# Kernel optimization log

Measured on AMD Instinct MI355X. Metric: run time of the kernel, lower is better.

The kernel has to match this reference:

```python
import jax, jax.numpy as jnp
import numpy as np

HEADS, DIM_HEAD = 8, 64
EPS = 1e-5  # torch InstanceNorm1d default


def instance_norm(t):
    # torch InstanceNorm1d(dim_head) applied to (b*h, n, d) normalizes over the
    # last dim d for each (b, h, n); affine=False, biased variance.
    mu = jnp.mean(t, axis=-1, keepdims=True)
    var = jnp.mean((t - mu) ** 2, axis=-1, keepdims=True)
    return (t - mu) * jax.lax.rsqrt(var + EPS)


def setup_inputs() -> dict:
    key = jax.random.key(0)
    k1, k2, k3, k4 = jax.random.split(key, 4)
    B, N, D = 8, 8192, 256
    inner = HEADS * DIM_HEAD  # 512
    x = jax.random.normal(k1, (B, N, D), jnp.float32)
    w_qkv = jax.random.normal(k2, (3 * inner, D), jnp.float32) / np.sqrt(D).astype(np.float32)
    w_out = jax.random.normal(k3, (D, inner), jnp.float32) / np.sqrt(inner).astype(np.float32)
    b_out = 0.01 * jax.random.normal(k4, (D,), jnp.float32)
    return {"x": x, "w_qkv": w_qkv, "w_out": w_out, "b_out": b_out}


def reference(x, w_qkv, w_out, b_out):
    B, N, _ = x.shape
    H, Dh = HEADS, DIM_HEAD
    # fused qkv projection: [B,N,3*H*Dh]
    qkv = jnp.einsum('bnd,ed->bne', x, w_qkv)
    q, k, v = jnp.split(qkv, 3, axis=-1)

    def to_heads(t):
        return t.reshape(B, N, H, Dh).transpose(0, 2, 1, 3)  # b h n d

    q, k, v = to_heads(q), to_heads(k), to_heads(v)
    # galerkin: instance-norm K and V
    k = instance_norm(k)
    v = instance_norm(v)
    # linear (non-softmax) attention: (K^T V) then Q @ (K^T V), scaled by 1/N
    dots = jnp.einsum('bhnd,bhne->bhde', k, v)            # [B,H,Dh,Dh]
    out = jnp.einsum('bhnd,bhde->bhne', q, dots) / N      # [B,H,N,Dh]
    out = out.transpose(0, 2, 1, 3).reshape(B, N, H * Dh)
    return jnp.einsum('bne,de->bnd', out, w_out) + b_out
```

## Files before the change

kernel.cpp:

```cpp
#include <hip/hip_runtime.h>
#include <hip/hip_bf16.h>
#include <stdint.h>

typedef __attribute__((ext_vector_type(8))) __bf16 bf16x8;
typedef __attribute__((ext_vector_type(8))) unsigned short ushort8_t;
typedef __attribute__((ext_vector_type(4))) unsigned short ushort4_t;
typedef __attribute__((ext_vector_type(4))) float f32x4;

#define MFMA16(a, b, c) __builtin_amdgcn_mfma_f32_16x16x32_bf16((a), (b), (c), 0, 0, 0)

static __device__ __forceinline__ unsigned short f2bf(float f) {
  union { float f; unsigned u; } v; v.f = f;
  unsigned r = v.u + 0x7fffu + ((v.u >> 16) & 1u);
  return (unsigned short)(r >> 16);
}
static __device__ __forceinline__ float bf2f(unsigned short u) {
  union { unsigned u; float f; } v; v.u = ((unsigned)u) << 16; return v.f;
}

static __device__ __forceinline__ void gld_lds16(const void* g, void* l) {
  __builtin_amdgcn_global_load_lds((const __attribute__((address_space(1))) void*)g,
                                   (__attribute__((address_space(3))) void*)l, 16, 0, 0);
}

__global__ __launch_bounds__(256) void k_convx(const float* __restrict__ x,
                                               unsigned short* __restrict__ xb) {
  size_t i = ((size_t)blockIdx.x * 256 + threadIdx.x) * 4;
  float4 v = *(const float4*)(x + i);
  ushort4_t o = { f2bf(v.x), f2bf(v.y), f2bf(v.z), f2bf(v.w) };
  *(ushort4_t*)(xb + i) = o;
}

__global__ void k_convw(const float* __restrict__ w, unsigned short* __restrict__ wb) {
  int i = (blockIdx.x * 256 + threadIdx.x) * 4;
  float4 v = *(const float4*)(w + i);
  ushort4_t o = { f2bf(v.x), f2bf(v.y), f2bf(v.z), f2bf(v.w) };
  *(ushort4_t*)(wb + i) = o;
}

__global__ void k_convo(const float* __restrict__ w, unsigned short* __restrict__ wb) {
  int i = (blockIdx.x * 256 + threadIdx.x) * 4;
  float4 v = *(const float4*)(w + i);
  ushort4_t o = { f2bf(v.x), f2bf(v.y), f2bf(v.z), f2bf(v.w) };
  *(ushort4_t*)(wb + i) = o;
}

__global__ __launch_bounds__(512) void k_fused(const unsigned short* __restrict__ xb,
                                               const unsigned short* __restrict__ wqb,
                                               float* __restrict__ partials) {
  __shared__ __align__(16) char smem[98304];
  unsigned short* As = (unsigned short*)smem;
  unsigned short* Bs = (unsigned short*)(smem + 65536);
  unsigned short* kt = (unsigned short*)smem;
  unsigned short* vt = (unsigned short*)(smem + 36864);

  const int t = threadIdx.x;
  const int w = t >> 6, lane = t & 63, lr = lane & 15, lg = lane >> 4;
  const int wr = w >> 1, wc = w & 1;

  const int id = blockIdx.x;
  const int nid = (id & 7) * 256 + (id >> 3);
  const int mt = nid >> 3, h = nid & 7;
  const long m0 = (long)mt * 256;

  const unsigned short* bk = wqb + (size_t)(512 + h * 64) * 256;
  const unsigned short* bv = wqb + (size_t)(1024 + h * 64) * 256;

  const int srl = t >> 3, sc = t & 7;
  const int swz = (sc ^ (srl & 7)) << 3;

#pragma unroll
  for (int i = 0; i < 4; ++i)
    gld_lds16(xb + (size_t)(m0 + i * 64 + srl) * 256 + swz, &As[i * 4096 + t * 8]);
  gld_lds16(bk + (size_t)srl * 256 + swz, &Bs[t * 8]);
  gld_lds16(bv + (size_t)srl * 256 + swz, &Bs[4096 + t * 8]);
  __syncthreads();

  f32x4 acc[4][4];
#pragma unroll
  for (int mb = 0; mb < 4; ++mb)
#pragma unroll
    for (int nb = 0; nb < 4; ++nb) acc[mb][nb] = f32x4{0.f, 0.f, 0.f, 0.f};

  for (int ks = 0; ks < 4; ++ks) {
    const int cur = ks & 1, nxt = cur ^ 1;
    if (ks < 3) {
      const int k0 = (ks + 1) * 64;
#pragma unroll
      for (int i = 0; i < 4; ++i)
        gld_lds16(xb + (size_t)(m0 + i * 64 + srl) * 256 + k0 + swz,
                  &As[nxt * 16384 + i * 4096 + t * 8]);
      gld_lds16(bk + (size_t)srl * 256 + k0 + swz, &Bs[nxt * 8192 + t * 8]);
      gld_lds16(bv + (size_t)srl * 256 + k0 + swz, &Bs[nxt * 8192 + 4096 + t * 8]);
    }
    bf16x8 a[4][2], b[4][2];
#pragma unroll
    for (int mb = 0; mb < 4; ++mb) {
      const int R = wr * 64 + mb * 16 + lr;
#pragma unroll
      for (int kh = 0; kh < 2; ++kh)
        a[mb][kh] = *(const bf16x8*)&As[cur * 16384 + R * 64 + ((((kh << 2) + lg) ^ (R & 7)) << 3)];
    }
#pragma unroll
    for (int nb = 0; nb < 4; ++nb) {
      const int E = wc * 64 + nb * 16 + lr;
#pragma unroll
      for (int kh = 0; kh < 2; ++kh)
        b[nb][kh] = *(const bf16x8*)&Bs[cur * 8192 + E * 64 + ((((kh << 2) + lg) ^ (E & 7)) << 3)];
    }
#pragma unroll
    for (int mb = 0; mb < 4; ++mb)
#pragma unroll
      for (int nb = 0; nb < 4; ++nb)
#pragma unroll
        for (int kh = 0; kh < 2; ++kh)
          acc[mb][nb] = MFMA16(a[mb][kh], b[nb][kh], acc[mb][nb]);
    __syncthreads();
  }

  unsigned short* dst = (wc == 0 ? kt : vt) + wr * 4608;
#pragma unroll
  for (int mb = 0; mb < 4; ++mb) {
#pragma unroll
    for (int rg = 0; rg < 4; ++rg) {
      float s1 = acc[mb][0][rg] + acc[mb][1][rg] + acc[mb][2][rg] + acc[mb][3][rg];
      float s2 = acc[mb][0][rg] * acc[mb][0][rg] + acc[mb][1][rg] * acc[mb][1][rg] +
                 acc[mb][2][rg] * acc[mb][2][rg] + acc[mb][3][rg] * acc[mb][3][rg];
      s1 += __shfl_xor(s1, 1); s2 += __shfl_xor(s2, 1);
      s1 += __shfl_xor(s1, 2); s2 += __shfl_xor(s2, 2);
      s1 += __shfl_xor(s1, 4); s2 += __shfl_xor(s2, 4);
      s1 += __shfl_xor(s1, 8); s2 += __shfl_xor(s2, 8);
      const float mean = s1 * (1.f / 64.f);
      const float rs = rsqrtf(s2 * (1.f / 64.f) - mean * mean + 1e-5f);
      const int nn = mb * 16 + lg * 4 + rg;
#pragma unroll
      for (int nb = 0; nb < 4; ++nb)
        dst[(nb * 16 + lr) * 72 + nn] = f2bf((acc[mb][nb][rg] - mean) * rs);
    }
  }
  __syncthreads();

  const int dblk = w >> 1, ep = w & 1;
  f32x4 acc2[2] = {f32x4{0.f, 0.f, 0.f, 0.f}, f32x4{0.f, 0.f, 0.f, 0.f}};
#pragma unroll
  for (int cn = 0; cn < 4; ++cn) {
#pragma unroll
    for (int ns = 0; ns < 64; ns += 32) {
      bf16x8 af = *(const bf16x8*)&kt[cn * 4608 + (dblk * 16 + lr) * 72 + ns + lg * 8];
#pragma unroll
      for (int e = 0; e < 2; ++e) {
        bf16x8 bvf = *(const bf16x8*)&vt[cn * 4608 + ((ep * 2 + e) * 16 + lr) * 72 + ns + lg * 8];
        acc2[e] = MFMA16(af, bvf, acc2[e]);
      }
    }
  }
  float* pb = partials + ((size_t)mt * 8 + h) * 4096;
#pragma unroll
  for (int e = 0; e < 2; ++e)
#pragma unroll
    for (int rg = 0; rg < 4; ++rg) {
      int d = dblk * 16 + lg * 4 + rg;
      int eo = (ep * 2 + e) * 16 + lr;
      pb[d * 64 + eo] = acc2[e][rg];
    }
}

__global__ __launch_bounds__(256) void k_mmat(const float* __restrict__ partials,
                                              const float* __restrict__ wqkv,
                                              unsigned short* __restrict__ tmpT) {
  __shared__ float dl[4096];
  __shared__ float wqls[64 * 256];
  const int bh = blockIdx.x, b = bh >> 3, h = bh & 7;
  const int t = threadIdx.x;
#pragma unroll
  for (int i = 0; i < 4; ++i) {
    int off = t * 16 + i * 4;
    f32x4 s = {0.f, 0.f, 0.f, 0.f};
    for (int c = 0; c < 32; ++c) {
      f32x4 p = *(const f32x4*)(partials + ((size_t)(b * 32 + c) * 8 + h) * 4096 + off);
      s += p;
    }
    *(f32x4*)&dl[off] = s;
  }
#pragma unroll
  for (int i = 0; i < 16; ++i) {
    int idx4 = i * 256 + t;
    int d = idx4 >> 6, c4 = idx4 & 63;
    *(f32x4*)&wqls[d * 256 + c4 * 4] =
        *(const f32x4*)(wqkv + (size_t)(h * 64 + d) * 256 + c4 * 4);
  }
  __syncthreads();
  const int k = t;
  const float scale = 1.0f / 8192.0f;
  float res[64];
  for (int e = 0; e < 64; ++e) {
    float s = 0.f;
#pragma unroll
    for (int d = 0; d < 64; ++d) s += dl[d * 64 + e] * wqls[d * 256 + k];
    res[e] = s * scale;
  }
  unsigned short* dstp = tmpT + (size_t)b * 131072 + (size_t)k * 512 + h * 64;
#pragma unroll
  for (int e8 = 0; e8 < 8; ++e8) {
    ushort8_t o;
#pragma unroll
    for (int j = 0; j < 8; ++j) o[j] = f2bf(res[e8 * 8 + j]);
    *(ushort8_t*)(dstp + e8 * 8) = o;
  }
}

__global__ __launch_bounds__(256) void k_pmat(const unsigned short* __restrict__ woutb,
                                              const unsigned short* __restrict__ tmpT,
                                              unsigned short* __restrict__ pswz) {
  const int bid = blockIdx.x;
  const int b = bid >> 2, oq = (bid >> 1) & 1, kq = bid & 1;
  const int t = threadIdx.x, w = t >> 6, lane = t & 63, lr = lane & 15, lg = lane >> 4;
  const int wr = w >> 1, wc = w & 1;
  const int ob = oq * 128 + wr * 64, kb = kq * 128 + wc * 64;
  const unsigned short* tb = tmpT + (size_t)b * 131072;

  f32x4 acc[4][4];
#pragma unroll
  for (int mb = 0; mb < 4; ++mb)
#pragma unroll
    for (int nb = 0; nb < 4; ++nb) acc[mb][nb] = f32x4{0.f, 0.f, 0.f, 0.f};

  for (int ks = 0; ks < 16; ++ks) {
    bf16x8 a[4], bb[4];
#pragma unroll
    for (int mb = 0; mb < 4; ++mb)
      a[mb] = *(const bf16x8*)(woutb + (size_t)(ob + mb * 16 + lr) * 512 + ks * 32 + lg * 8);
#pragma unroll
    for (int nb = 0; nb < 4; ++nb)
      bb[nb] = *(const bf16x8*)(tb + (size_t)(kb + nb * 16 + lr) * 512 + ks * 32 + lg * 8);
#pragma unroll
    for (int mb = 0; mb < 4; ++mb)
#pragma unroll
      for (int nb = 0; nb < 4; ++nb) acc[mb][nb] = MFMA16(a[mb], bb[nb], acc[mb][nb]);
  }

  unsigned short* pb = pswz + (size_t)b * 65536;
#pragma unroll
  for (int mb = 0; mb < 4; ++mb)
#pragma unroll
    for (int nb = 0; nb < 4; ++nb)
#pragma unroll
      for (int rg = 0; rg < 4; ++rg) {
        int o = ob + mb * 16 + lg * 4 + rg;
        int k = kb + nb * 16 + lr;
        pb[(((k >> 5) * 16 + (o >> 4)) * 64 + (o & 15) + ((k >> 3) & 3) * 16) * 8 + (k & 7)] =
            f2bf(acc[mb][nb][rg]);
      }
}

__global__ __launch_bounds__(512) void k_gemm2(const unsigned short* __restrict__ xb,
                                               const unsigned short* __restrict__ pswz,
                                               const float* __restrict__ bout,
                                               float* __restrict__ out) {
  __shared__ unsigned short As[2][128 * 64];
  const int b = blockIdx.x >> 6, mt = blockIdx.x & 63;
  const long m0 = (long)mt * 128;
  const int t = threadIdx.x, w = t >> 6, lane = t & 63, lr = lane & 15, lg = lane >> 4;
  const int wr = w >> 2, wc = w & 3;
  const unsigned short* qb = xb + ((size_t)b * 8192 + m0) * 256;
  const unsigned short* Mb = pswz + (size_t)b * 65536;
  const int srl = lane >> 3, sc = lane & 7;

#pragma unroll
  for (int i = 0; i < 2; ++i) {
    const int row = (i * 8 + w) * 8 + srl;
    gld_lds16(qb + (size_t)row * 256 + ((sc ^ (row & 7)) << 3),
              &As[0][(i * 8 + w) * 512]);
  }
  __syncthreads();

  f32x4 acc[4][4];
#pragma unroll
  for (int mb = 0; mb < 4; ++mb)
#pragma unroll
    for (int nb = 0; nb < 4; ++nb) acc[mb][nb] = f32x4{0.f, 0.f, 0.f, 0.f};

  for (int ks = 0; ks < 4; ++ks) {
    const int cur = ks & 1, nxt = cur ^ 1;
    if (ks < 3) {
      const int k0 = (ks + 1) * 64;
#pragma unroll
      for (int i = 0; i < 2; ++i) {
        const int row = (i * 8 + w) * 8 + srl;
        gld_lds16(qb + (size_t)row * 256 + k0 + ((sc ^ (row & 7)) << 3),
                  &As[nxt][(i * 8 + w) * 512]);
      }
    }
    bf16x8 a[4][2], bfr[2][4];
#pragma unroll
    for (int mb = 0; mb < 4; ++mb) {
      const int R = wr * 64 + mb * 16 + lr;
#pragma unroll
      for (int kh = 0; kh < 2; ++kh)
        a[mb][kh] = *(const bf16x8*)&As[cur][R * 64 + ((((kh << 2) + lg) ^ (R & 7)) << 3)];
    }
#pragma unroll
    for (int kh = 0; kh < 2; ++kh)
#pragma unroll
      for (int nb = 0; nb < 4; ++nb)
        bfr[kh][nb] = *(const bf16x8*)(Mb + ((((size_t)ks * 2 + kh) * 16 + wc * 4 + nb) * 64 + lane) * 8);
#pragma unroll
    for (int mb = 0; mb < 4; ++mb)
#pragma unroll
      for (int nb = 0; nb < 4; ++nb)
#pragma unroll
        for (int kh = 0; kh < 2; ++kh)
          acc[mb][nb] = MFMA16(a[mb][kh], bfr[kh][nb], acc[mb][nb]);
    __syncthreads();
  }

  float bo[4];
#pragma unroll
  for (int nb = 0; nb < 4; ++nb) bo[nb] = bout[wc * 64 + nb * 16 + lr];
  float* ob = out + ((size_t)b * 8192 + m0) * 256;
#pragma unroll
  for (int mb = 0; mb < 4; ++mb)
#pragma unroll
    for (int nb = 0; nb < 4; ++nb)
#pragma unroll
      for (int rg = 0; rg < 4; ++rg) {
        int row = wr * 64 + mb * 16 + lg * 4 + rg;
        int c = wc * 64 + nb * 16 + lr;
        ob[(size_t)row * 256 + c] = acc[mb][nb][rg] + bo[nb];
      }
}

extern "C" void kernel_launch(void* const* d_in, const int* in_sizes, int n_in,
                              void* d_out, int out_size, void* d_ws, size_t ws_size,
                              hipStream_t stream) {
  const float* x    = (const float*)d_in[0];
  const float* wqkv = (const float*)d_in[1];
  const float* wout = (const float*)d_in[2];
  const float* bout = (const float*)d_in[3];
  float* out = (float*)d_out;

  char* ws = (char*)d_ws;
  unsigned short* xb = (unsigned short*)ws;
  size_t off = (size_t)65536 * 256 * 2;
  unsigned short* wqb = (unsigned short*)(ws + off);
  off += (size_t)1536 * 256 * 2;
  unsigned short* woutb = (unsigned short*)(ws + off);
  off += (size_t)256 * 512 * 2;
  float* partials = (float*)(ws + off);
  off += (size_t)2048 * 4096 * 4;
  unsigned short* tmpT = (unsigned short*)(ws + off);
  off += (size_t)8 * 131072 * 2;
  unsigned short* pswz = (unsigned short*)(ws + off);
  off += (size_t)8 * 65536 * 2;

  k_convx<<<16384, 256, 0, stream>>>(x, xb);
  k_convw<<<384, 256, 0, stream>>>(wqkv, wqb);
  k_convo<<<128, 256, 0, stream>>>(wout, woutb);
  k_fused<<<2048, 512, 0, stream>>>(xb, wqb, partials);
  k_mmat<<<64, 256, 0, stream>>>(partials, wqkv, tmpT);
  k_pmat<<<32, 256, 0, stream>>>(woutb, tmpT, pswz);
  k_gemm2<<<512, 512, 0, stream>>>(xb, pswz, bout, out);
}
```

Baseline: 169.8 us.

## Make fused K/V projection persistent with 256x256 tiles over two heads

The fused K/V projection kernel now computes a 256x256 output tile (K and V for two heads) per block and loops over four row chunks, launching 256 blocks instead of 2048. Each block keeps its running K^T V accumulator in registers and writes one partial per chunk group, which cuts partial traffic and the reduction work in k_mmat. The k-loop is split into four MFMA phases, with barriers, setprio and staggered async global-to-LDS loads to overlap memory and compute. The cost is 144KB of LDS, more accumulator registers, and fewer blocks, which may reduce occupancy and load balance.

```diff
diff --git a/kernel.cpp b/kernel.cpp
--- a/kernel.cpp
+++ b/kernel.cpp
@@ -48,120 +48,215 @@
 __global__ __launch_bounds__(512) void k_fused(const unsigned short* __restrict__ xb,
                                                const unsigned short* __restrict__ wqb,
                                                float* __restrict__ partials) {
-  __shared__ __align__(16) char smem[98304];
+  __shared__ __align__(16) char smem[147456];
   unsigned short* As = (unsigned short*)smem;
   unsigned short* Bs = (unsigned short*)(smem + 65536);
-  unsigned short* kt = (unsigned short*)smem;
-  unsigned short* vt = (unsigned short*)(smem + 36864);
+  unsigned short* tt = (unsigned short*)smem;
 
   const int t = threadIdx.x;
   const int w = t >> 6, lane = t & 63, lr = lane & 15, lg = lane >> 4;
-  const int wr = w >> 1, wc = w & 1;
+  const int wr = w >> 2, wc = w & 3;
+  const int hh = w >> 2, dblk = w & 3;
 
   const int id = blockIdx.x;
-  const int nid = (id & 7) * 256 + (id >> 3);
-  const int mt = nid >> 3, h = nid & 7;
-  const long m0 = (long)mt * 256;
-
-  const unsigned short* bk = wqb + (size_t)(512 + h * 64) * 256;
-  const unsigned short* bv = wqb + (size_t)(1024 + h * 64) * 256;
-
-  const int srl = t >> 3, sc = t & 7;
-  const int swz = (sc ^ (srl & 7)) << 3;
-
-#pragma unroll
-  for (int i = 0; i < 4; ++i)
-    gld_lds16(xb + (size_t)(m0 + i * 64 + srl) * 256 + swz, &As[i * 4096 + t * 8]);
-  gld_lds16(bk + (size_t)srl * 256 + swz, &Bs[t * 8]);
-  gld_lds16(bv + (size_t)srl * 256 + swz, &Bs[4096 + t * 8]);
-  __syncthreads();
-
-  f32x4 acc[4][4];
-#pragma unroll
-  for (int mb = 0; mb < 4; ++mb)
-#pragma unroll
-    for (int nb = 0; nb < 4; ++nb) acc[mb][nb] = f32x4{0.f, 0.f, 0.f, 0.f};
-
-  for (int ks = 0; ks < 4; ++ks) {
-    const int cur = ks & 1, nxt = cur ^ 1;
-    if (ks < 3) {
-      const int k0 = (ks + 1) * 64;
-#pragma unroll
-      for (int i = 0; i < 4; ++i)
-        gld_lds16(xb + (size_t)(m0 + i * 64 + srl) * 256 + k0 + swz,
-                  &As[nxt * 16384 + i * 4096 + t * 8]);
-      gld_lds16(bk + (size_t)srl * 256 + k0 + swz, &Bs[nxt * 8192 + t * 8]);
-      gld_lds16(bv + (size_t)srl * 256 + k0 + swz, &Bs[nxt * 8192 + 4096 + t * 8]);
-    }
-    bf16x8 a[4][2], b[4][2];
-#pragma unroll
-    for (int mb = 0; mb < 4; ++mb) {
-      const int R = wr * 64 + mb * 16 + lr;
-#pragma unroll
-      for (int kh = 0; kh < 2; ++kh)
-        a[mb][kh] = *(const bf16x8*)&As[cur * 16384 + R * 64 + ((((kh << 2) + lg) ^ (R & 7)) << 3)];
-    }
-#pragma unroll
-    for (int nb = 0; nb < 4; ++nb) {
-      const int E = wc * 64 + nb * 16 + lr;
-#pragma unroll
-      for (int kh = 0; kh < 2; ++kh)
-        b[nb][kh] = *(const bf16x8*)&Bs[cur * 8192 + E * 64 + ((((kh << 2) + lg) ^ (E & 7)) << 3)];
-    }
-#pragma unroll
-    for (int mb = 0; mb < 4; ++mb)
-#pragma unroll
-      for (int nb = 0; nb < 4; ++nb)
+  const int nid = (id & 7) * 32 + (id >> 3);
+  const int mg = nid >> 2, hp = nid & 3;
+
+  const int srl = lane >> 3, sc = lane & 7;
+
+  int aoff[2][2];
+  const unsigned short* bptr[2][2];
+#pragma unroll
+  for (int i = 0; i < 2; ++i) {
+    const int r = (w * 2 + i) * 8 + srl;
+    const int swz = (sc ^ (r & 7)) << 3;
+#pragma unroll
+    for (int H = 0; H < 2; ++H) {
+      const int br = H * 128 + r;
+      const int grp = br >> 6;
+      const int grow = ((grp & 1) ? 1024 : 512) +
+                       ((grp >> 1) ? (hp + 4) * 64 : hp * 64) + (br & 63);
+      bptr[H][i] = wqb + (size_t)grow * 256 + swz;
+      aoff[H][i] = (H * 128 + r) * 256 + swz;
+    }
+  }
+
+  f32x4 acc2[4];
+#pragma unroll
+  for (int nb = 0; nb < 4; ++nb) acc2[nb] = f32x4{0.f, 0.f, 0.f, 0.f};
+
+  for (int mi = 0; mi < 4; ++mi) {
+    const long m0 = ((long)mg * 4 + mi) * 256;
+    const unsigned short* am = xb + (size_t)m0 * 256;
+
+#pragma unroll
+    for (int i = 0; i < 2; ++i) {
+      gld_lds16(am + aoff[0][i], &As[(w * 2 + i) * 512]);
+      gld_lds16(am + aoff[1][i], &As[8192 + (w * 2 + i) * 512]);
+      gld_lds16(bptr[0][i],      &Bs[(w * 2 + i) * 512]);
+      gld_lds16(bptr[1][i],      &Bs[8192 + (w * 2 + i) * 512]);
+    }
+    __syncthreads();
+
+    f32x4 acc[8][4];
+#pragma unroll
+    for (int i = 0; i < 8; ++i)
+#pragma unroll
+      for (int j = 0; j < 4; ++j) acc[i][j] = f32x4{0.f, 0.f, 0.f, 0.f};
+
+    bf16x8 a[4][2], b[2][2][2];
+
+    for (int kt = 0; kt < 4; ++kt) {
+      const int cur = kt & 1, nxt = cur ^ 1;
+      const int kn0 = (kt + 1) * 64;
+      const bool st = kt < 3;
+
+#pragma unroll
+      for (int mb = 0; mb < 4; ++mb) {
+        const int R = wr * 128 + mb * 16 + lr;
 #pragma unroll
         for (int kh = 0; kh < 2; ++kh)
-          acc[mb][nb] = MFMA16(a[mb][kh], b[nb][kh], acc[mb][nb]);
+          a[mb][kh] = *(const bf16x8*)&As[cur * 16384 + R * 64 + ((((kh << 2) + lg) ^ (R & 7)) << 3)];
+      }
+#pragma unroll
+      for (int nb = 0; nb < 2; ++nb) {
+        const int E = wc * 64 + nb * 16 + lr;
+#pragma unroll
+        for (int kh = 0; kh < 2; ++kh)
+          b[0][nb][kh] = *(const bf16x8*)&Bs[cur * 16384 + E * 64 + ((((kh << 2) + lg) ^ (E & 7)) << 3)];
+      }
+      if (st) {
+#pragma unroll
+        for (int i = 0; i < 2; ++i)
+          gld_lds16(am + aoff[0][i] + kn0, &As[nxt * 16384 + (w * 2 + i) * 512]);
+      }
+      __builtin_amdgcn_s_barrier();
+      __builtin_amdgcn_s_setprio(1);
+#pragma unroll
+      for (int mb = 0; mb < 4; ++mb)
+#pragma unroll
+        for (int nb = 0; nb < 2; ++nb)
+#pragma unroll
+          for (int kh = 0; kh < 2; ++kh)
+            acc[mb][nb] = MFMA16(a[mb][kh], b[0][nb][kh], acc[mb][nb]);
+      __builtin_amdgcn_s_setprio(0);
+      __builtin_amdgcn_s_barrier();
+
+#pragma unroll
+      for (int nb = 0; nb < 2; ++nb) {
+        const int E = wc * 64 + 32 + nb * 16 + lr;
+#pragma unroll
+        for (int kh = 0; kh < 2; ++kh)
+          b[1][nb][kh] = *(const bf16x8*)&Bs[cur * 16384 + E * 64 + ((((kh << 2) + lg) ^ (E & 7)) << 3)];
+      }
+      if (st) {
+#pragma unroll
+        for (int i = 0; i < 2; ++i)
+          gld_lds16(am + aoff[1][i] + kn0, &As[nxt * 16384 + 8192 + (w * 2 + i) * 512]);
+      }
+      __builtin_amdgcn_s_barrier();
+      __builtin_amdgcn_s_setprio(1);
+#pragma unroll
+      for (int mb = 0; mb < 4; ++mb)
+#pragma unroll
+        for (int nb = 0; nb < 2; ++nb)
+#pragma unroll
+          for (int kh = 0; kh < 2; ++kh)
+            acc[mb][2 + nb] = MFMA16(a[mb][kh], b[1][nb][kh], acc[mb][2 + nb]);
+      __builtin_amdgcn_s_setprio(0);
+      __builtin_amdgcn_s_barrier();
+
+#pragma unroll
+      for (int mb = 0; mb < 4; ++mb) {
+        const int R = wr * 128 + 64 + mb * 16 + lr;
+#pragma unroll
+        for (int kh = 0; kh < 2; ++kh)
+          a[mb][kh] = *(const bf16x8*)&As[cur * 16384 + R * 64 + ((((kh << 2) + lg) ^ (R & 7)) << 3)];
+      }
+      if (st) {
+#pragma unroll
+        for (int i = 0; i < 2; ++i)
+          gld_lds16(bptr[0][i] + kn0, &Bs[nxt * 16384 + (w * 2 + i) * 512]);
+      }
+      __builtin_amdgcn_s_barrier();
+      __builtin_amdgcn_s_setprio(1);
+#pragma unroll
+      for (int mb = 0; mb < 4; ++mb)
+#pragma unroll
+        for (int nb = 0; nb < 2; ++nb)
+#pragma unroll
+          for (int kh = 0; kh < 2; ++kh)
+            acc[4 + mb][nb] = MFMA16(a[mb][kh], b[0][nb][kh], acc[4 + mb][nb]);
+      __builtin_amdgcn_s_setprio(0);
+      __builtin_amdgcn_s_barrier();
+
+      if (st) {
+#pragma unroll
+        for (int i = 0; i < 2; ++i)
+          gld_lds16(bptr[1][i] + kn0, &Bs[nxt * 16384 + 8192 + (w * 2 + i) * 512]);
+      }
+      __builtin_amdgcn_s_barrier();
+      __builtin_amdgcn_s_setprio(1);
+#pragma unroll
+      for (int mb = 0; mb < 4; ++mb)
+#pragma unroll
+        for (int nb = 0; nb < 2; ++nb)
+#pragma unroll
+          for (int kh = 0; kh < 2; ++kh)
+            acc[4 + mb][2 + nb] = MFMA16(a[mb][kh], b[1][nb][kh], acc[4 + mb][2 + nb]);
+      __builtin_amdgcn_s_setprio(0);
+      __syncthreads();
+    }
+
+    unsigned short* dst = tt + (size_t)wc * 18432;
+#pragma unroll
+    for (int i = 0; i < 8; ++i) {
+      const int cn = wr * 2 + (i >> 2);
+      const int mb = i & 3;
+#pragma unroll
+      for (int rg = 0; rg < 4; ++rg) {
+        float s1 = acc[i][0][rg] + acc[i][1][rg] + acc[i][2][rg] + acc[i][3][rg];
+        float s2 = acc[i][0][rg] * acc[i][0][rg] + acc[i][1][rg] * acc[i][1][rg] +
+                   acc[i][2][rg] * acc[i][2][rg] + acc[i][3][rg] * acc[i][3][rg];
+        s1 += __shfl_xor(s1, 1); s2 += __shfl_xor(s2, 1);
+        s1 += __shfl_xor(s1, 2); s2 += __shfl_xor(s2, 2);
+        s1 += __shfl_xor(s1, 4); s2 += __shfl_xor(s2, 4);
+        s1 += __shfl_xor(s1, 8); s2 += __shfl_xor(s2, 8);
+        const float mean = s1 * (1.f / 64.f);
+        const float rs = rsqrtf(s2 * (1.f / 64.f) - mean * mean + 1e-5f);
+        const int nn = mb * 16 + lg * 4 + rg;
+#pragma unroll
+        for (int nb = 0; nb < 4; ++nb)
+          dst[cn * 4608 + (nb * 16 + lr) * 72 + nn] = f2bf((acc[i][nb][rg] - mean) * rs);
+      }
+    }
     __syncthreads();
-  }
-
-  unsigned short* dst = (wc == 0 ? kt : vt) + wr * 4608;
-#pragma unroll
-  for (int mb = 0; mb < 4; ++mb) {
+
+    const unsigned short* ktp = tt + (size_t)(hh * 2) * 18432;
+    const unsigned short* vtp = tt + (size_t)(hh * 2 + 1) * 18432;
+#pragma unroll
+    for (int cn = 0; cn < 4; ++cn) {
+#pragma unroll
+      for (int ns = 0; ns < 64; ns += 32) {
+        bf16x8 af = *(const bf16x8*)&ktp[cn * 4608 + (dblk * 16 + lr) * 72 + ns + lg * 8];
+#pragma unroll
+        for (int nb = 0; nb < 4; ++nb) {
+          bf16x8 bv = *(const bf16x8*)&vtp[cn * 4608 + (nb * 16 + lr) * 72 + ns + lg * 8];
+          acc2[nb] = MFMA16(af, bv, acc2[nb]);
+        }
+      }
+    }
+    __syncthreads();
+  }
+
+  float* pb = partials + (((size_t)mg * 4 + hp) * 2 + hh) * 4096;
+#pragma unroll
+  for (int nb = 0; nb < 4; ++nb)
 #pragma unroll
     for (int rg = 0; rg < 4; ++rg) {
-      float s1 = acc[mb][0][rg] + acc[mb][1][rg] + acc[mb][2][rg] + acc[mb][3][rg];
-      float s2 = acc[mb][0][rg] * acc[mb][0][rg] + acc[mb][1][rg] * acc[mb][1][rg] +
-                 acc[mb][2][rg] * acc[mb][2][rg] + acc[mb][3][rg] * acc[mb][3][rg];
-      s1 += __shfl_xor(s1, 1); s2 += __shfl_xor(s2, 1);
-      s1 += __shfl_xor(s1, 2); s2 += __shfl_xor(s2, 2);
-      s1 += __shfl_xor(s1, 4); s2 += __shfl_xor(s2, 4);
-      s1 += __shfl_xor(s1, 8); s2 += __shfl_xor(s2, 8);
-      const float mean = s1 * (1.f / 64.f);
-      const float rs = rsqrtf(s2 * (1.f / 64.f) - mean * mean + 1e-5f);
-      const int nn = mb * 16 + lg * 4 + rg;
-#pragma unroll
-      for (int nb = 0; nb < 4; ++nb)
-        dst[(nb * 16 + lr) * 72 + nn] = f2bf((acc[mb][nb][rg] - mean) * rs);
-    }
-  }
-  __syncthreads();
-
-  const int dblk = w >> 1, ep = w & 1;
-  f32x4 acc2[2] = {f32x4{0.f, 0.f, 0.f, 0.f}, f32x4{0.f, 0.f, 0.f, 0.f}};
-#pragma unroll
-  for (int cn = 0; cn < 4; ++cn) {
-#pragma unroll
-    for (int ns = 0; ns < 64; ns += 32) {
-      bf16x8 af = *(const bf16x8*)&kt[cn * 4608 + (dblk * 16 + lr) * 72 + ns + lg * 8];
-#pragma unroll
-      for (int e = 0; e < 2; ++e) {
-        bf16x8 bvf = *(const bf16x8*)&vt[cn * 4608 + ((ep * 2 + e) * 16 + lr) * 72 + ns + lg * 8];
-        acc2[e] = MFMA16(af, bvf, acc2[e]);
-      }
-    }
-  }
-  float* pb = partials + ((size_t)mt * 8 + h) * 4096;
-#pragma unroll
-  for (int e = 0; e < 2; ++e)
-#pragma unroll
-    for (int rg = 0; rg < 4; ++rg) {
-      int d = dblk * 16 + lg * 4 + rg;
-      int eo = (ep * 2 + e) * 16 + lr;
-      pb[d * 64 + eo] = acc2[e][rg];
+      const int d = dblk * 16 + lg * 4 + rg;
+      const int e = nb * 16 + lr;
+      pb[d * 64 + e] = acc2[nb][rg];
     }
 }
 
@@ -176,8 +271,9 @@
   for (int i = 0; i < 4; ++i) {
     int off = t * 16 + i * 4;
     f32x4 s = {0.f, 0.f, 0.f, 0.f};
-    for (int c = 0; c < 32; ++c) {
-      f32x4 p = *(const f32x4*)(partials + ((size_t)(b * 32 + c) * 8 + h) * 4096 + off);
+    for (int c = 0; c < 8; ++c) {
+      const size_t chunk = ((size_t)(b * 8 + c) * 4 + (h & 3)) * 2 + (h >> 2);
+      f32x4 p = *(const f32x4*)(partials + chunk * 4096 + off);
       s += p;
     }
     *(f32x4*)&dl[off] = s;
@@ -347,7 +443,7 @@
   unsigned short* woutb = (unsigned short*)(ws + off);
   off += (size_t)256 * 512 * 2;
   float* partials = (float*)(ws + off);
-  off += (size_t)2048 * 4096 * 4;
+  off += (size_t)512 * 4096 * 4;
   unsigned short* tmpT = (unsigned short*)(ws + off);
   off += (size_t)8 * 131072 * 2;
   unsigned short* pswz = (unsigned short*)(ws + off);
@@ -356,7 +452,7 @@
   k_convx<<<16384, 256, 0, stream>>>(x, xb);
   k_convw<<<384, 256, 0, stream>>>(wqkv, wqb);
   k_convo<<<128, 256, 0, stream>>>(wout, woutb);
-  k_fused<<<2048, 512, 0, stream>>>(xb, wqb, partials);
+  k_fused<<<256, 512, 0, stream>>>(xb, wqb, partials);
   k_mmat<<<64, 256, 0, stream>>>(partials, wqkv, tmpT);
   k_pmat<<<32, 256, 0, stream>>>(woutb, tmpT, pswz);
   k_gemm2<<<512, 512, 0, stream>>>(xb, pswz, bout, out);
```

Result: slower. 190.0 us (+11.9%).

## Shrink fused K/V projection tile to 128 rows and loop over four subtiles

Applied to the files above, without the earlier changes.

The fused K/V projection plus K^T V kernel now processes 128-row tiles in a loop of four per block, instead of one 256-row tile. It accumulates the K^T V partial across iterations. Shared memory drops from 96KB to 64KB and accumulator registers halve, which should allow more blocks per CU. The partials buffer and the k_mmat reduction shrink to 16 chunks per batch. In exchange each block runs a serialized loop with extra barriers, and weight tiles are reloaded every iteration.

```diff
diff --git a/kernel.cpp b/kernel.cpp
--- a/kernel.cpp
+++ b/kernel.cpp
@@ -48,119 +48,133 @@
 __global__ __launch_bounds__(512) void k_fused(const unsigned short* __restrict__ xb,
                                                const unsigned short* __restrict__ wqb,
                                                float* __restrict__ partials) {
-  __shared__ __align__(16) char smem[98304];
+  __shared__ __align__(16) char smem[65536];
   unsigned short* As = (unsigned short*)smem;
-  unsigned short* Bs = (unsigned short*)(smem + 65536);
+  unsigned short* Bs = (unsigned short*)(smem + 32768);
   unsigned short* kt = (unsigned short*)smem;
-  unsigned short* vt = (unsigned short*)(smem + 36864);
+  unsigned short* vt = (unsigned short*)(smem + 18432);
 
   const int t = threadIdx.x;
   const int w = t >> 6, lane = t & 63, lr = lane & 15, lg = lane >> 4;
   const int wr = w >> 1, wc = w & 1;
+  const int dblk = w >> 1, ep = w & 1;
 
   const int id = blockIdx.x;
-  const int nid = (id & 7) * 256 + (id >> 3);
-  const int mt = nid >> 3, h = nid & 7;
-  const long m0 = (long)mt * 256;
-
-  const unsigned short* bk = wqb + (size_t)(512 + h * 64) * 256;
-  const unsigned short* bv = wqb + (size_t)(1024 + h * 64) * 256;
-
-  const int srl = t >> 3, sc = t & 7;
-  const int swz = (sc ^ (srl & 7)) << 3;
-
-#pragma unroll
-  for (int i = 0; i < 4; ++i)
-    gld_lds16(xb + (size_t)(m0 + i * 64 + srl) * 256 + swz, &As[i * 4096 + t * 8]);
-  gld_lds16(bk + (size_t)srl * 256 + swz, &Bs[t * 8]);
-  gld_lds16(bv + (size_t)srl * 256 + swz, &Bs[4096 + t * 8]);
-  __syncthreads();
-
-  f32x4 acc[4][4];
-#pragma unroll
-  for (int mb = 0; mb < 4; ++mb)
-#pragma unroll
-    for (int nb = 0; nb < 4; ++nb) acc[mb][nb] = f32x4{0.f, 0.f, 0.f, 0.f};
-
-  for (int ks = 0; ks < 4; ++ks) {
-    const int cur = ks & 1, nxt = cur ^ 1;
-    if (ks < 3) {
-      const int k0 = (ks + 1) * 64;
-#pragma unroll
-      for (int i = 0; i < 4; ++i)
-        gld_lds16(xb + (size_t)(m0 + i * 64 + srl) * 256 + k0 + swz,
-                  &As[nxt * 16384 + i * 4096 + t * 8]);
-      gld_lds16(bk + (size_t)srl * 256 + k0 + swz, &Bs[nxt * 8192 + t * 8]);
-      gld_lds16(bv + (size_t)srl * 256 + k0 + swz, &Bs[nxt * 8192 + 4096 + t * 8]);
-    }
-    bf16x8 a[4][2], b[4][2];
-#pragma unroll
-    for (int mb = 0; mb < 4; ++mb) {
-      const int R = wr * 64 + mb * 16 + lr;
-#pragma unroll
-      for (int kh = 0; kh < 2; ++kh)
-        a[mb][kh] = *(const bf16x8*)&As[cur * 16384 + R * 64 + ((((kh << 2) + lg) ^ (R & 7)) << 3)];
-    }
-#pragma unroll
-    for (int nb = 0; nb < 4; ++nb) {
-      const int E = wc * 64 + nb * 16 + lr;
-#pragma unroll
-      for (int kh = 0; kh < 2; ++kh)
-        b[nb][kh] = *(const bf16x8*)&Bs[cur * 8192 + E * 64 + ((((kh << 2) + lg) ^ (E & 7)) << 3)];
-    }
-#pragma unroll
-    for (int mb = 0; mb < 4; ++mb)
-#pragma unroll
-      for (int nb = 0; nb < 4; ++nb)
+  const int nid = (id & 7) * 128 + (id >> 3);
+  const int mg = nid >> 3, h = nid & 7;
+
+  const int srl = lane >> 3, sc = lane & 7;
+  const int swz = (sc ^ srl) << 3;
+
+  const unsigned short* bptr[2];
+  int aoff[2];
+#pragma unroll
+  for (int i = 0; i < 2; ++i) {
+    const int br = (w * 2 + i) * 8 + srl;
+    const int grow = (br < 64) ? (512 + h * 64 + br) : (1024 + h * 64 + (br - 64));
+    bptr[i] = wqb + (size_t)grow * 256 + swz;
+    aoff[i] = br * 256 + swz;
+  }
+
+  f32x4 acc2[2] = {f32x4{0.f, 0.f, 0.f, 0.f}, f32x4{0.f, 0.f, 0.f, 0.f}};
+
+  for (int mi = 0; mi < 4; ++mi) {
+    const long m0 = ((long)mg * 4 + mi) * 128;
+    const unsigned short* am = xb + (size_t)m0 * 256;
+
+#pragma unroll
+    for (int i = 0; i < 2; ++i) {
+      gld_lds16(am + aoff[i], &As[(w * 2 + i) * 512]);
+      gld_lds16(bptr[i],      &Bs[(w * 2 + i) * 512]);
+    }
+    __syncthreads();
+
+    f32x4 acc[2][4];
+#pragma unroll
+    for (int mb = 0; mb < 2; ++mb)
+#pragma unroll
+      for (int nb = 0; nb < 4; ++nb) acc[mb][nb] = f32x4{0.f, 0.f, 0.f, 0.f};
+
+    for (int ktt = 0; ktt < 4; ++ktt) {
+      const int cur = ktt & 1, nxt = cur ^ 1;
+      if (ktt < 3) {
+        const int k0 = (ktt + 1) * 64;
+#pragma unroll
+        for (int i = 0; i < 2; ++i) {
+          gld_lds16(am + aoff[i] + k0, &As[nxt * 8192 + (w * 2 + i) * 512]);
+          gld_lds16(bptr[i] + k0,      &Bs[nxt * 8192 + (w * 2 + i) * 512]);
+        }
+      }
+      bf16x8 a[2][2], b[4][2];
+#pragma unroll
+      for (int mb = 0; mb < 2; ++mb) {
+        const int R = wr * 32 + mb * 16 + lr;
 #pragma unroll
         for (int kh = 0; kh < 2; ++kh)
-          acc[mb][nb] = MFMA16(a[mb][kh], b[nb][kh], acc[mb][nb]);
+          a[mb][kh] = *(const bf16x8*)&As[cur * 8192 + R * 64 + ((((kh << 2) + lg) ^ (R & 7)) << 3)];
+      }
+#pragma unroll
+      for (int nb = 0; nb < 4; ++nb) {
+        const int E = wc * 64 + nb * 16 + lr;
+#pragma unroll
+        for (int kh = 0; kh < 2; ++kh)
+          b[nb][kh] = *(const bf16x8*)&Bs[cur * 8192 + E * 64 + ((((kh << 2) + lg) ^ (E & 7)) << 3)];
+      }
+#pragma unroll
+      for (int mb = 0; mb < 2; ++mb)
+#pragma unroll
+        for (int nb = 0; nb < 4; ++nb)
+#pragma unroll
+          for (int kh = 0; kh < 2; ++kh)
+            acc[mb][nb] = MFMA16(a[mb][kh], b[nb][kh], acc[mb][nb]);
+      __syncthreads();
+    }
+
+    unsigned short* dst = (wc == 0) ? kt : vt;
+#pragma unroll
+    for (int mb = 0; mb < 2; ++mb) {
+#pragma unroll
+      for (int rg = 0; rg < 4; ++rg) {
+        float s1 = acc[mb][0][rg] + acc[mb][1][rg] + acc[mb][2][rg] + acc[mb][3][rg];
+        float s2 = acc[mb][0][rg] * acc[mb][0][rg] + acc[mb][1][rg] * acc[mb][1][rg] +
+                   acc[mb][2][rg] * acc[mb][2][rg] + acc[mb][3][rg] * acc[mb][3][rg];
+        s1 += __shfl_xor(s1, 1); s2 += __shfl_xor(s2, 1);
+        s1 += __shfl_xor(s1, 2); s2 += __shfl_xor(s2, 2);
+        s1 += __shfl_xor(s1, 4); s2 += __shfl_xor(s2, 4);
+        s1 += __shfl_xor(s1, 8); s2 += __shfl_xor(s2, 8);
+        const float mean = s1 * (1.f / 64.f);
+        const float rs = rsqrtf(s2 * (1.f / 64.f) - mean * mean + 1e-5f);
+        const int n = wr * 32 + mb * 16 + lg * 4 + rg;
+        const int cn = n >> 6, nn = n & 63;
+#pragma unroll
+        for (int nb = 0; nb < 4; ++nb)
+          dst[cn * 4608 + (nb * 16 + lr) * 72 + nn] = f2bf((acc[mb][nb][rg] - mean) * rs);
+      }
+    }
     __syncthreads();
-  }
-
-  unsigned short* dst = (wc == 0 ? kt : vt) + wr * 4608;
-#pragma unroll
-  for (int mb = 0; mb < 4; ++mb) {
+
+#pragma unroll
+    for (int cn = 0; cn < 2; ++cn) {
+#pragma unroll
+      for (int ns = 0; ns < 64; ns += 32) {
+        bf16x8 af = *(const bf16x8*)&kt[cn * 4608 + (dblk * 16 + lr) * 72 + ns + lg * 8];
+#pragma unroll
+        for (int e = 0; e < 2; ++e) {
+          bf16x8 bv = *(const bf16x8*)&vt[cn * 4608 + ((ep * 2 + e) * 16 + lr) * 72 + ns + lg * 8];
+          acc2[e] = MFMA16(af, bv, acc2[e]);
+        }
+      }
+    }
+    __syncthreads();
+  }
+
+  float* pb = partials + ((size_t)mg * 8 + h) * 4096;
+#pragma unroll
+  for (int e = 0; e < 2; ++e)
 #pragma unroll
     for (int rg = 0; rg < 4; ++rg) {
-      float s1 = acc[mb][0][rg] + acc[mb][1][rg] + acc[mb][2][rg] + acc[mb][3][rg];
-      float s2 = acc[mb][0][rg] * acc[mb][0][rg] + acc[mb][1][rg] * acc[mb][1][rg] +
-                 acc[mb][2][rg] * acc[mb][2][rg] + acc[mb][3][rg] * acc[mb][3][rg];
-      s1 += __shfl_xor(s1, 1); s2 += __shfl_xor(s2, 1);
-      s1 += __shfl_xor(s1, 2); s2 += __shfl_xor(s2, 2);
-      s1 += __shfl_xor(s1, 4); s2 += __shfl_xor(s2, 4);
-      s1 += __shfl_xor(s1, 8); s2 += __shfl_xor(s2, 8);
-      const float mean = s1 * (1.f / 64.f);
-      const float rs = rsqrtf(s2 * (1.f / 64.f) - mean * mean + 1e-5f);
-      const int nn = mb * 16 + lg * 4 + rg;
-#pragma unroll
-      for (int nb = 0; nb < 4; ++nb)
-        dst[(nb * 16 + lr) * 72 + nn] = f2bf((acc[mb][nb][rg] - mean) * rs);
-    }
-  }
-  __syncthreads();
-
-  const int dblk = w >> 1, ep = w & 1;
-  f32x4 acc2[2] = {f32x4{0.f, 0.f, 0.f, 0.f}, f32x4{0.f, 0.f, 0.f, 0.f}};
-#pragma unroll
-  for (int cn = 0; cn < 4; ++cn) {
-#pragma unroll
-    for (int ns = 0; ns < 64; ns += 32) {
-      bf16x8 af = *(const bf16x8*)&kt[cn * 4608 + (dblk * 16 + lr) * 72 + ns + lg * 8];
-#pragma unroll
-      for (int e = 0; e < 2; ++e) {
-        bf16x8 bvf = *(const bf16x8*)&vt[cn * 4608 + ((ep * 2 + e) * 16 + lr) * 72 + ns + lg * 8];
-        acc2[e] = MFMA16(af, bvf, acc2[e]);
-      }
-    }
-  }
-  float* pb = partials + ((size_t)mt * 8 + h) * 4096;
-#pragma unroll
-  for (int e = 0; e < 2; ++e)
-#pragma unroll
-    for (int rg = 0; rg < 4; ++rg) {
-      int d = dblk * 16 + lg * 4 + rg;
-      int eo = (ep * 2 + e) * 16 + lr;
+      const int d = dblk * 16 + lg * 4 + rg;
+      const int eo = (ep * 2 + e) * 16 + lr;
       pb[d * 64 + eo] = acc2[e][rg];
     }
 }
@@ -176,8 +190,9 @@
   for (int i = 0; i < 4; ++i) {
     int off = t * 16 + i * 4;
     f32x4 s = {0.f, 0.f, 0.f, 0.f};
-    for (int c = 0; c < 32; ++c) {
-      f32x4 p = *(const f32x4*)(partials + ((size_t)(b * 32 + c) * 8 + h) * 4096 + off);
+    for (int c = 0; c < 16; ++c) {
+      const size_t chunk = (size_t)(b * 16 + c) * 8 + h;
+      f32x4 p = *(const f32x4*)(partials + chunk * 4096 + off);
       s += p;
     }
     *(f32x4*)&dl[off] = s;
@@ -347,7 +362,7 @@
   unsigned short* woutb = (unsigned short*)(ws + off);
   off += (size_t)256 * 512 * 2;
   float* partials = (float*)(ws + off);
-  off += (size_t)2048 * 4096 * 4;
+  off += (size_t)1024 * 4096 * 4;
   unsigned short* tmpT = (unsigned short*)(ws + off);
   off += (size_t)8 * 131072 * 2;
   unsigned short* pswz = (unsigned short*)(ws + off);
@@ -356,7 +371,7 @@
   k_convx<<<16384, 256, 0, stream>>>(x, xb);
   k_convw<<<384, 256, 0, stream>>>(wqkv, wqb);
   k_convo<<<128, 256, 0, stream>>>(wout, woutb);
-  k_fused<<<2048, 512, 0, stream>>>(xb, wqb, partials);
+  k_fused<<<1024, 512, 0, stream>>>(xb, wqb, partials);
   k_mmat<<<64, 256, 0, stream>>>(partials, wqkv, tmpT);
   k_pmat<<<32, 256, 0, stream>>>(woutb, tmpT, pswz);
   k_gemm2<<<512, 512, 0, stream>>>(xb, pswz, bout, out);
```

After: 166.0 us. 2.2% less time.
